# Kernel tuning notes

Hardware: AMD Instinct MI355X
Metric: run time of the kernel (lower is better)

Reference implementation:

```python
import jax, jax.numpy as jnp
import numpy as np

GN_EPS = 1e-5
NN_EPS = 1e-8


def _three_nn_interpolate(xyz1, xyz2, points2):
    # xyz1: (B,N,3), xyz2: (B,M,3), points2: (B,M,C) -> (B,N,C)
    src_sq = jnp.sum(xyz1 ** 2, axis=-1, keepdims=True)          # (B,N,1)
    dst_sq = jnp.sum(xyz2 ** 2, axis=-1)[:, None, :]             # (B,1,M)
    inner = jnp.einsum('bnd,bmd->bnm', xyz1, xyz2)               # (B,N,M)
    dist = src_sq - 2.0 * inner + dst_sq                         # (B,N,M)
    neg_d, idx = jax.lax.top_k(-dist, 3)                         # (B,N,3)
    d = -neg_d
    inv = 1.0 / (d + NN_EPS)
    w = inv / jnp.sum(inv, axis=-1, keepdims=True)               # (B,N,3)
    grouped = jax.vmap(lambda p, i: p[i])(points2, idx)          # (B,N,3,C)
    return jnp.sum(grouped * w[..., None], axis=2)               # (B,N,C)


def _group_norm(x, weight, bias, groups):
    # x: (B,C,N)
    B, C, N = x.shape
    xg = x.reshape(B, groups, C // groups, N)
    mu = jnp.mean(xg, axis=(2, 3), keepdims=True)
    var = jnp.var(xg, axis=(2, 3), keepdims=True)
    xg = (xg - mu) * jax.lax.rsqrt(var + GN_EPS)
    x = xg.reshape(B, C, N)
    return x * weight[None, :, None] + bias[None, :, None]


def setup_inputs() -> dict:
    key = jax.random.key(0)
    ks = jax.random.split(key, 10)
    B, N, M, C1, C2 = 8, 8192, 2048, 128, 256
    mlp = [256, 128]
    in_ch = C1 + C2
    inp = {
        'xyz1': jax.random.normal(ks[0], (B, N, 3), dtype=jnp.float32),
        'xyz2': jax.random.normal(ks[1], (B, M, 3), dtype=jnp.float32),
        'points1': jax.random.normal(ks[2], (B, N, C1), dtype=jnp.float32),
        'points2': jax.random.normal(ks[3], (B, M, C2), dtype=jnp.float32),
        'w0': jax.random.normal(ks[4], (mlp[0], in_ch), dtype=jnp.float32) * (1.0 / np.sqrt(in_ch)),
        'w1': jax.random.normal(ks[5], (mlp[1], mlp[0]), dtype=jnp.float32) * (1.0 / np.sqrt(mlp[0])),
        'gn0_w': jnp.ones((mlp[0],), dtype=jnp.float32),
        'gn0_b': jnp.zeros((mlp[0],), dtype=jnp.float32),
        'gn1_w': jnp.ones((mlp[1],), dtype=jnp.float32),
        'gn1_b': jnp.zeros((mlp[1],), dtype=jnp.float32),
    }
    return inp


def reference(xyz1, xyz2, points1, points2, w0, w1, gn0_w, gn0_b, gn1_w, gn1_b):
    interpolated = _three_nn_interpolate(xyz1, xyz2, points2)    # (B,N,C2)
    feat = jnp.concatenate([points1, interpolated], axis=-1)     # (B,N,C1+C2)
    # conv1d kernel size 1 == pointwise matmul; work in (B,C,N) layout for GN
    h = jnp.einsum('bnc,oc->bon', feat, w0)                      # (B,256,N)
    h = jax.nn.relu(_group_norm(h, gn0_w, gn0_b, groups=min(32, w0.shape[0])))
    h = jnp.einsum('bcn,oc->bon', h, w1)                         # (B,128,N)
    h = jax.nn.relu(_group_norm(h, gn1_w, gn1_b, groups=min(32, w1.shape[0])))
    return jnp.transpose(h, (0, 2, 1))                           # (B,N,128)
```

## Files before the change

kernel.cpp:

```cpp
#include <hip/hip_runtime.h>


#define DEVI __device__ __forceinline__

static constexpr int B  = 8;
static constexpr int N  = 8192;
static constexpr int M  = 2048;
static constexpr int C1 = 128;
static constexpr int C2 = 256;
static constexpr int CIN = C1 + C2;
static constexpr int H0 = 256;
static constexpr int H1 = 128;
static constexpr int BN = B * N;
static constexpr int NSEG = 8;
static constexpr int SEGL = M / NSEG;

typedef __bf16 bf16x8 __attribute__((ext_vector_type(8)));
typedef float  f32x4  __attribute__((ext_vector_type(4)));
typedef unsigned short ushort8v __attribute__((ext_vector_type(8)));

DEVI float bf2f(unsigned short u) {
    union { unsigned int i; float f; } v; v.i = ((unsigned int)u) << 16; return v.f;
}
DEVI unsigned short f2bf(float f) {
    union { float f; unsigned int i; } v; v.f = f;
    unsigned int x = v.i;
    return (unsigned short)((x + 0x7fffu + ((x >> 16) & 1u)) >> 16);
}
DEVI float ldin(const void* p, size_t i, int bf) {
    return bf ? bf2f(((const unsigned short*)p)[i]) : ((const float*)p)[i];
}
DEVI void ld8(const void* p, size_t i, int bf, float r[8]) {
    if (bf) {
        const ushort8v u = *(const ushort8v*)((const unsigned short*)p + i);
#pragma unroll
        for (int k = 0; k < 8; k++) r[k] = bf2f(u[k]);
    } else {
        const float4 a = *(const float4*)((const float*)p + i);
        const float4 b = *(const float4*)((const float*)p + i + 4);
        r[0] = a.x; r[1] = a.y; r[2] = a.z; r[3] = a.w;
        r[4] = b.x; r[5] = b.y; r[6] = b.z; r[7] = b.w;
    }
}
DEVI void ld8b(const unsigned short* p, size_t i, float r[8]) {
    const ushort8v u = *(const ushort8v*)(p + i);
#pragma unroll
    for (int k = 0; k < 8; k++) r[k] = bf2f(u[k]);
}

DEVI void gload16(const void* g, void* l) {
    __builtin_amdgcn_global_load_lds(
        (const __attribute__((address_space(1))) void*)g,
        (__attribute__((address_space(3))) void*)l, 16, 0, 0);
}

__global__ __launch_bounds__(64) void detect_dtype_kernel(const void* __restrict__ xyz1,
                                                          int* __restrict__ flag)
{
    const unsigned short* u = (const unsigned short*)xyz1;
    const int lane = threadIdx.x;
    const float av = fabsf(bf2f(u[2 * lane]));
    const bool in_range = (av >= 1e-4f && av <= 100.0f);
    const unsigned long long m = __ballot(in_range);
    if (lane == 0) flag[0] = (__popcll(m) >= 32) ? 1 : 0;
}

DEVI void cvt8(const void* src, unsigned short* dst, size_t j8, int bf) {
    if (bf) {
        *(ushort8v*)(dst + j8 * 8) = *(const ushort8v*)((const unsigned short*)src + j8 * 8);
    } else {
        float r[8];
        ld8(src, j8 * 8, 0, r);
        ushort8v o;
#pragma unroll
        for (int k = 0; k < 8; k++) o[k] = f2bf(r[k]);
        *(ushort8v*)(dst + j8 * 8) = o;
    }
}

__global__ __launch_bounds__(256) void prep_kernel(
    const void* __restrict__ w0, const void* __restrict__ w1,
    const void* __restrict__ p2, const void* __restrict__ xyz2,
    unsigned short* __restrict__ w0b, unsigned short* __restrict__ w1b,
    unsigned short* __restrict__ pb2,
    float4* __restrict__ c4, float* __restrict__ partz,
    const int* __restrict__ flag)
{
    const int bf = flag[0];
    constexpr int R0 = H0 * CIN / 8;
    constexpr int R1 = H1 * H0 / 8;
    constexpr int R2 = B * M;
    constexpr int R4 = B * M * C2 / 8;
    constexpr int R5 = 1024;
    constexpr int TOT = R0 + R1 + R2 + R4 + R5;
    for (int i = blockIdx.x * blockDim.x + threadIdx.x; i < TOT; i += gridDim.x * blockDim.x) {
        int j = i;
        if (j < R0) { cvt8(w0, w0b, j, bf); continue; }
        j -= R0;
        if (j < R1) { cvt8(w1, w1b, j, bf); continue; }
        j -= R1;
        if (j < R2) {
            const float x = ldin(xyz2, (size_t)j * 3 + 0, bf);
            const float y = ldin(xyz2, (size_t)j * 3 + 1, bf);
            const float z = ldin(xyz2, (size_t)j * 3 + 2, bf);
            const float sq = __fadd_rn(__fadd_rn(__fmul_rn(x, x), __fmul_rn(y, y)), __fmul_rn(z, z));
            c4[j] = make_float4(x, y, z, 0.5f * sq);
            continue;
        }
        j -= R2;
        if (j < R4) { cvt8(p2, pb2, j, bf); continue; }
        j -= R4;
        partz[j] = 0.f;
    }
}

__global__ __launch_bounds__(256) void knn3_split_kernel(
    const void* __restrict__ xyz1, const float4* __restrict__ c4,
    int* __restrict__ ci, const int* __restrict__ flag)
{
    const int bf = flag[0];
    const int tid = threadIdx.x;
    const int gid = blockIdx.x * 256 + tid;
    const int s = blockIdx.y;
    const int b = __builtin_amdgcn_readfirstlane(gid >> 13);

    const float x1 = ldin(xyz1, (size_t)gid * 3 + 0, bf);
    const float y1 = ldin(xyz1, (size_t)gid * 3 + 1, bf);
    const float z1 = ldin(xyz1, (size_t)gid * 3 + 2, bf);

    const float4* __restrict__ cand = c4 + b * M + s * SEGL;
    const int jbase = s * SEGL;
    constexpr int HALF = SEGL / 2;

    float a0 = 3.4e38f, a1 = 3.4e38f, a2 = 3.4e38f;
    int   ia0 = 0, ia1 = 0, ia2 = 0;
    float g0 = 3.4e38f, g1 = 3.4e38f, g2 = 3.4e38f;
    int   ig0 = 0, ig1 = 0, ig2 = 0;

#pragma unroll 4
    for (int j = 0; j < HALF; ++j) {
        const float4 pA = cand[j];
        const float4 pB = cand[j + HALF];
        const float sA = __builtin_fmaf(-x1, pA.x,
                          __builtin_fmaf(-y1, pA.y,
                           __builtin_fmaf(-z1, pA.z, pA.w)));
        const float sB = __builtin_fmaf(-x1, pB.x,
                          __builtin_fmaf(-y1, pB.y,
                           __builtin_fmaf(-z1, pB.z, pB.w)));
        {
            const int jn = jbase + j;
            const bool c0 = sA < a0;
            const float t1 = fmaxf(sA, a0); a0 = fminf(sA, a0);
            const int  tj1 = c0 ? ia0 : jn; ia0 = c0 ? jn : ia0;
            const bool c1 = t1 < a1;
            const float t2 = fmaxf(t1, a1); a1 = fminf(t1, a1);
            const int  tj2 = c1 ? ia1 : tj1; ia1 = c1 ? tj1 : ia1;
            const bool c2 = t2 < a2;
            a2 = fminf(t2, a2); ia2 = c2 ? tj2 : ia2;
        }
        {
            const int jn = jbase + HALF + j;
            const bool c0 = sB < g0;
            const float t1 = fmaxf(sB, g0); g0 = fminf(sB, g0);
            const int  tj1 = c0 ? ig0 : jn; ig0 = c0 ? jn : ig0;
            const bool c1 = t1 < g1;
            const float t2 = fmaxf(t1, g1); g1 = fminf(t1, g1);
            const int  tj2 = c1 ? ig1 : tj1; ig1 = c1 ? tj1 : ig1;
            const bool c2 = t2 < g2;
            g2 = fminf(t2, g2); ig2 = c2 ? tj2 : ig2;
        }
    }

    float mv[3] = { g0, g1, g2 };
    int   mi[3] = { ig0, ig1, ig2 };
#pragma unroll
    for (int k = 0; k < 3; ++k) {
        const float sv = mv[k]; const int jn = mi[k];
        const bool c0 = sv < a0;
        const float t1 = fmaxf(sv, a0); a0 = fminf(sv, a0);
        const int  tj1 = c0 ? ia0 : jn; ia0 = c0 ? jn : ia0;
        const bool c1 = t1 < a1;
        const float t2 = fmaxf(t1, a1); a1 = fminf(t1, a1);
        const int  tj2 = c1 ? ia1 : tj1; ia1 = c1 ? tj1 : ia1;
        const bool c2 = t2 < a2;
        a2 = fminf(t2, a2); ia2 = c2 ? tj2 : ia2;
    }

    ci[(size_t)(s * 3 + 0) * BN + gid] = ia0;
    ci[(size_t)(s * 3 + 1) * BN + gid] = ia1;
    ci[(size_t)(s * 3 + 2) * BN + gid] = ia2;
}

__global__ __launch_bounds__(512, 4) void gemm1_kernel(
    const void* __restrict__ p1, const unsigned short* __restrict__ pb2,
    const void* __restrict__ xyz1, const float4* __restrict__ c4,
    const int* __restrict__ ci,
    const unsigned short* __restrict__ W,
    unsigned short* __restrict__ h0, float2* __restrict__ part,
    const int* __restrict__ flag)
{
    constexpr int K = CIN;
    constexpr int COUT = H0;
    __shared__ __align__(16) char lds[81920];

    const int bf = flag[0];
    const int t = threadIdx.x;
    const int l = t & 63;
    const int w = t >> 6;
    const int qbase = blockIdx.x * 64;
    const int b = qbase >> 13;

    float* dd = (float*)(lds + 49152);
    int*   di = (int*)(lds + 55296);
    int*   sidx = (int*)(lds + 61440);
    float* sw = (float*)(lds + 62208);

    {
        const int ql = t >> 3;
        const int q  = qbase + ql;
        const int kk0 = (t & 7) * 3;
        const float x1 = ldin(xyz1, (size_t)q * 3 + 0, bf);
        const float y1 = ldin(xyz1, (size_t)q * 3 + 1, bf);
        const float z1 = ldin(xyz1, (size_t)q * 3 + 2, bf);
        const float sq1 = __fadd_rn(__fadd_rn(__fmul_rn(x1, x1), __fmul_rn(y1, y1)), __fmul_rn(z1, z1));
#pragma unroll
        for (int u = 0; u < 3; ++u) {
            const int k = kk0 + u;
            const int ix = ci[(size_t)k * BN + q];
            const float4 p = c4[b * M + ix];
            const float inner = __fadd_rn(__fadd_rn(__fmul_rn(x1, p.x), __fmul_rn(y1, p.y)),
                                          __fmul_rn(z1, p.z));
            const float pw2 = p.w + p.w;
            const float d = __fadd_rn(__fsub_rn(sq1, __fmul_rn(2.0f, inner)), pw2);
            dd[ql * 24 + k] = d;
            di[ql * 24 + k] = ix;
        }
    }
    __syncthreads();

    if (t < 64) {
        float bd0 = 3.4e38f, bd1 = 3.4e38f, bd2 = 3.4e38f;
        int   bi0 = 0x7fffffff, bi1 = 0x7fffffff, bi2 = 0x7fffffff;
#pragma unroll
        for (int k = 0; k < 24; ++k) {
            const float d  = dd[t * 24 + k];
            const int   ix = di[t * 24 + k];
            const bool lt2 = (d < bd2) || (d == bd2 && ix < bi2);
            if (lt2) {
                const bool lt0 = (d < bd0) || (d == bd0 && ix < bi0);
                const bool lt1 = (d < bd1) || (d == bd1 && ix < bi1);
                if (lt0)      { bd2 = bd1; bi2 = bi1; bd1 = bd0; bi1 = bi0; bd0 = d; bi0 = ix; }
                else if (lt1) { bd2 = bd1; bi2 = bi1; bd1 = d; bi1 = ix; }
                else          { bd2 = d; bi2 = ix; }
            }
        }
        const float v0 = 1.0f / (bd0 + 1e-8f);
        const float v1 = 1.0f / (bd1 + 1e-8f);
        const float v2 = 1.0f / (bd2 + 1e-8f);
        const float s = v0 + v1 + v2;
        sidx[t * 3 + 0] = bi0; sidx[t * 3 + 1] = bi1; sidx[t * 3 + 2] = bi2;
        sw[t * 3 + 0] = v0 / s; sw[t * 3 + 1] = v1 / s; sw[t * 3 + 2] = v2 / s;
    }
    __syncthreads();

#pragma unroll 1
    for (int it = 0; it < 6; ++it) {
        const int task = it * 512 + t;
        const int ql = task / 48;
        const int c8 = task % 48;
        const int c  = c8 * 8;
        float v[8];
        if (c < C1) {
            ld8(p1, (size_t)(qbase + ql) * C1 + c, bf, v);
        } else {
            const int c2 = c - C1;
            float t0[8], t1[8], t2[8];
            ld8b(pb2, (size_t)(b * M + sidx[ql * 3 + 0]) * C2 + c2, t0);
            ld8b(pb2, (size_t)(b * M + sidx[ql * 3 + 1]) * C2 + c2, t1);
            ld8b(pb2, (size_t)(b * M + sidx[ql * 3 + 2]) * C2 + c2, t2);
            const float w0v = sw[ql * 3 + 0], w1v = sw[ql * 3 + 1], w2v = sw[ql * 3 + 2];
#pragma unroll
            for (int k = 0; k < 8; k++) v[k] = w0v * t0[k] + w1v * t1[k] + w2v * t2[k];
        }
        ushort8v o;
#pragma unroll
        for (int k = 0; k < 8; k++) o[k] = f2bf(v[k]);
        *(ushort8v*)(lds + ql * 768 + ((c8 >> 3) << 7) + ((((c8 & 7) ^ (ql & 7)) << 4))) = o;
    }
    __syncthreads();

    const int srow  = l >> 3;
    const int sslot = l & 7;
    const int wr  = w >> 2;
    const int wc  = w & 3;
    const int rl  = l & 15;
    const int kq  = l >> 4;
    const int swz7 = l & 7;

    f32x4 acc[2][4];
#pragma unroll
    for (int i = 0; i < 2; i++)
#pragma unroll
        for (int j = 0; j < 4; j++) acc[i][j] = (f32x4)0.0f;

    int aoff[2], boff[4];
#pragma unroll
    for (int i = 0; i < 2; i++) aoff[i] = (wr * 32 + i * 16 + rl) * 768;
#pragma unroll
    for (int j = 0; j < 4; j++) boff[j] = 49152 + (wc * 64 + j * 16 + rl) * 128;

    constexpr int NT = K / 64;

#pragma unroll 1
    for (int tt = 0; tt < NT; ++tt) {
        const int k0 = tt * 64;
#pragma unroll
        for (int i = 0; i < 4; ++i) {
            const int cb = w * 4 + i;
            const int rb = cb * 8 + srow;
            const int ke = (sslot ^ (rb & 7)) << 3;
            gload16(W + ((size_t)rb * K + k0 + ke), lds + 49152 + cb * 1024);
        }
        __syncthreads();
#pragma unroll
        for (int ks = 0; ks < 2; ++ks) {
            const int akb = (tt << 7) + (((ks * 4 + kq) ^ swz7) << 4);
            const int bkb = (ks * 64 + kq * 16) ^ (swz7 << 4);
            bf16x8 af[2], bfr[4];
#pragma unroll
            for (int i = 0; i < 2; i++) af[i]  = *(const bf16x8*)(lds + aoff[i] + akb);
#pragma unroll
            for (int j = 0; j < 4; j++) bfr[j] = *(const bf16x8*)(lds + boff[j] + bkb);
#pragma unroll
            for (int i = 0; i < 2; i++)
#pragma unroll
                for (int j = 0; j < 4; j++)
                    acc[i][j] = __builtin_amdgcn_mfma_f32_16x16x32_bf16(af[i], bfr[j], acc[i][j], 0, 0, 0);
        }
        __syncthreads();
    }

    const int crow = qbase + wr * 32 + kq * 4;
    const int ccol = wc * 64 + rl;
    float gsum[4], gss[4];
#pragma unroll
    for (int j = 0; j < 4; j++) {
        float s = 0.f, ss = 0.f;
#pragma unroll
        for (int i = 0; i < 2; i++)
#pragma unroll
            for (int r = 0; r < 4; r++) {
                const unsigned short hb = f2bf(acc[i][j][r]);
                h0[(size_t)(crow + i * 16 + r) * COUT + ccol + j * 16] = hb;
                const float x = bf2f(hb);
                s += x; ss += x * x;
            }
        gsum[j] = s; gss[j] = ss;
    }
    __syncthreads();
    float2* sred = (float2*)lds;
    if (t < 32) sred[t] = make_float2(0.f, 0.f);
    __syncthreads();
#pragma unroll
    for (int j = 0; j < 4; j++) {
        const int g = wc * 8 + j * 2 + (rl >> 3);
        atomicAdd(&sred[g].x, gsum[j]);
        atomicAdd(&sred[g].y, gss[j]);
    }
    __syncthreads();
    if (t < 32) {
        atomicAdd(&part[b * 32 + t].x, sred[t].x);
        atomicAdd(&part[b * 32 + t].y, sred[t].y);
    }
}

__global__ __launch_bounds__(256) void gemm2_kernel(
    const unsigned short* __restrict__ h0, const float2* __restrict__ part0,
    const void* __restrict__ gw, const void* __restrict__ gb,
    const unsigned short* __restrict__ W,
    unsigned short* __restrict__ h1, float2* __restrict__ part1,
    const int* __restrict__ flag)
{
    constexpr int K = H0;
    constexpr int COUT = H1;
    __shared__ __align__(16) char lds[32768];
    __shared__ float2 stlds[32];

    const int bf = flag[0];
    const int tid = threadIdx.x;
    const int l   = tid & 63;
    const int w   = tid >> 6;
    const int rowBase = blockIdx.x * 128;
    const int b = rowBase >> 13;

    if (tid < 32) {
        const float2 p = part0[b * 32 + tid];
        const float cnt = (float)N * 8.0f;
        const float mu  = p.x / cnt;
        const float var = p.y / cnt - mu * mu;
        stlds[tid] = make_float2(mu, rsqrtf(var + 1e-5f));
    }
    __syncthreads();

    const int srow  = l >> 3;
    const int sslot = l & 7;

    f32x4 acc[4][4];
#pragma unroll
    for (int i = 0; i < 4; i++)
#pragma unroll
        for (int j = 0; j < 4; j++) acc[i][j] = (f32x4)0.0f;

    const int wr  = (tid >> 7) & 1;
    const int wc  = (tid >> 6) & 1;
    const int rl  = l & 15;
    const int kq  = l >> 4;
    const int swz = (l & 7) << 4;
    int aoff[4], boff[4];
#pragma unroll
    for (int i = 0; i < 4; i++) {
        aoff[i] = (wr * 64 + i * 16 + rl) * 128;
        boff[i] = 16384 + (wc * 64 + i * 16 + rl) * 128;
    }

    constexpr int NT = K / 64;

#pragma unroll 1
    for (int t = 0; t < NT; ++t) {
        const int k0 = t * 64;
#pragma unroll
        for (int i = 0; i < 4; ++i) {
            const int cb = w * 4 + i;
            const int r  = cb * 8 + srow;
            const int ke = (sslot ^ (r & 7)) << 3;
            gload16(W + ((size_t)r * K + k0 + ke), lds + 16384 + cb * 1024);
        }
#pragma unroll
        for (int i = 0; i < 4; ++i) {
            const int r = (w * 4 + i) * 8 + srow;
            const int kslot = sslot ^ (r & 7);
            const int c = k0 + (kslot << 3);
            const float2 ms = stlds[c >> 3];
            float gwv[8], gbv[8];
            ld8(gw, c, bf, gwv);
            ld8(gb, c, bf, gbv);
            const ushort8v hv = *(const ushort8v*)(h0 + (size_t)(rowBase + r) * H0 + c);
            ushort8v o;
#pragma unroll
            for (int k = 0; k < 8; k++) {
                const float x = bf2f(hv[k]);
                o[k] = f2bf(fmaxf((x - ms.x) * ms.y * gwv[k] + gbv[k], 0.f));
            }
            *(ushort8v*)(lds + r * 128 + (sslot << 4)) = o;
        }
        __syncthreads();
#pragma unroll
        for (int ks = 0; ks < 2; ++ks) {
            const int kb = (ks * 64 + kq * 16) ^ swz;
            bf16x8 af[4], bfr[4];
#pragma unroll
            for (int i = 0; i < 4; i++) af[i]  = *(const bf16x8*)(lds + aoff[i] + kb);
#pragma unroll
            for (int j = 0; j < 4; j++) bfr[j] = *(const bf16x8*)(lds + boff[j] + kb);
#pragma unroll
            for (int i = 0; i < 4; i++)
#pragma unroll
                for (int j = 0; j < 4; j++)
                    acc[i][j] = __builtin_amdgcn_mfma_f32_16x16x32_bf16(af[i], bfr[j], acc[i][j], 0, 0, 0);
        }
        __syncthreads();
    }

    const int crow = rowBase + wr * 64 + kq * 4;
    const int ccol = wc * 64 + rl;
    float gsum[4], gss[4];
#pragma unroll
    for (int j = 0; j < 4; j++) {
        float s = 0.f, ss = 0.f;
#pragma unroll
        for (int i = 0; i < 4; i++)
#pragma unroll
            for (int r = 0; r < 4; r++) {
                const unsigned short hb = f2bf(acc[i][j][r]);
                h1[(size_t)(crow + i * 16 + r) * COUT + ccol + j * 16] = hb;
                const float x = bf2f(hb);
                s += x; ss += x * x;
            }
        gsum[j] = s; gss[j] = ss;
    }
    __syncthreads();
    float2* sred = (float2*)lds;
    if (tid < 32) sred[tid] = make_float2(0.f, 0.f);
    __syncthreads();
#pragma unroll
    for (int j = 0; j < 4; j++) {
        const int g = wc * 16 + j * 4 + (rl >> 2);
        atomicAdd(&sred[g].x, gsum[j]);
        atomicAdd(&sred[g].y, gss[j]);
    }
    __syncthreads();
    if (tid < 32) {
        atomicAdd(&part1[b * 32 + tid].x, sred[tid].x);
        atomicAdd(&part1[b * 32 + tid].y, sred[tid].y);
    }
}

__global__ __launch_bounds__(256) void gn_norm_relu_kernel(
    const unsigned short* __restrict__ h, const float2* __restrict__ part1,
    const void* __restrict__ gw, const void* __restrict__ gb,
    void* __restrict__ out, const int* __restrict__ flag)
{
    constexpr int C = H1;
    constexpr int cpg = 4;
    constexpr int C4 = C >> 2;
    constexpr int total4 = BN * C / 4;

    __shared__ float2 stlds[256];
    {
        const float2 p = part1[threadIdx.x];
        const float cnt = (float)N * (float)cpg;
        const float mu  = p.x / cnt;
        const float var = p.y / cnt - mu * mu;
        stlds[threadIdx.x] = make_float2(mu, rsqrtf(var + 1e-5f));
    }
    __syncthreads();

    const int bf = flag[0];
    for (int i4 = blockIdx.x * blockDim.x + threadIdx.x; i4 < total4; i4 += gridDim.x * blockDim.x) {
        const int c = (i4 % C4) * 4;
        const int p = i4 / C4;
        const int b = p >> 13;
        const float2 ms = stlds[b * 32 + c / cpg];
        const ushort4 hv = *(const ushort4*)(h + (size_t)i4 * 4);
        float r[4] = { bf2f(hv.x), bf2f(hv.y), bf2f(hv.z), bf2f(hv.w) };
#pragma unroll
        for (int k = 0; k < 4; k++) {
            const float gwv = ldin(gw, c + k, bf);
            const float gbv = ldin(gb, c + k, bf);
            r[k] = fmaxf((r[k] - ms.x) * ms.y * gwv + gbv, 0.f);
        }
        if (bf) {
            ushort4 o;
            o.x = f2bf(r[0]); o.y = f2bf(r[1]); o.z = f2bf(r[2]); o.w = f2bf(r[3]);
            *(ushort4*)((unsigned short*)out + (size_t)i4 * 4) = o;
        } else {
            float4 o; o.x = r[0]; o.y = r[1]; o.z = r[2]; o.w = r[3];
            *(float4*)((float*)out + (size_t)i4 * 4) = o;
        }
    }
}

extern "C" void kernel_launch(void* const* d_in, const int* in_sizes, int n_in,
                              void* d_out, int out_size, void* d_ws, size_t ws_size,
                              hipStream_t stream)
{
    const void* xyz1    = d_in[0];
    const void* xyz2    = d_in[1];
    const void* points1 = d_in[2];
    const void* points2 = d_in[3];
    const void* w0      = d_in[4];
    const void* w1      = d_in[5];
    const void* gn0w    = d_in[6];
    const void* gn0b    = d_in[7];
    const void* gn1w    = d_in[8];
    const void* gn1b    = d_in[9];

    char* ws = (char*)d_ws;
    unsigned short* h0     = (unsigned short*)ws;
    unsigned short* h1     = (unsigned short*)(ws + 33554432);
    unsigned short* w0b    = (unsigned short*)(ws + 50331648);
    unsigned short* w1b    = (unsigned short*)(ws + 50528256);
    unsigned short* pb2    = (unsigned short*)(ws + 50593792);
    float4*         c4     = (float4*)(ws + 58982400);
    int*            ci     = (int*)(ws + 59244544);
    float2*         part0  = (float2*)(ws + 65536000);
    float2*         part1  = (float2*)(ws + 65538048);
    int*            flag   = (int*)(ws + 65540096);

    detect_dtype_kernel<<<1, 64, 0, stream>>>(xyz1, flag);

    prep_kernel<<<1024, 256, 0, stream>>>(w0, w1, points2, xyz2,
                                          w0b, w1b, pb2, c4, (float*)part0, flag);

    {
        dim3 g(BN / 256, NSEG);
        knn3_split_kernel<<<g, 256, 0, stream>>>(xyz1, c4, ci, flag);
    }

    gemm1_kernel<<<BN / 64, 512, 0, stream>>>(points1, pb2, xyz1, c4, ci,
                                              w0b, h0, part0, flag);

    gemm2_kernel<<<BN / 128, 256, 0, stream>>>(h0, part0, gn0w, gn0b, w1b, h1,
                                               part1, flag);

    gn_norm_relu_kernel<<<1024, 256, 0, stream>>>(h1, part1, gn1w, gn1b, d_out, flag);
}
```

Before: 294.1 us.

## Gather fp32 points2 directly, inline dtype detection, widen gemm1 blocks to 1024 threads

Drops the prep-pass conversion of points2 to bf16. gemm1 now gathers and weights the three neighbours straight from the original fp32 buffer, which avoids a full read and write pass over points2 but doubles the bytes fetched per gather. The separate dtype-detection kernel is removed and each kernel runs the ballot check itself, saving one launch. gemm1 is retiled to 1024 threads (16 waves, each holding a 16x64 output tile), which halves per-wave accumulator registers and raises the thread count available for the gather, and the prep grid is shrunk to match its smaller workload.

```diff
diff --git a/kernel.cpp b/kernel.cpp
--- a/kernel.cpp
+++ b/kernel.cpp
@@ -42,27 +42,20 @@
         r[4] = b.x; r[5] = b.y; r[6] = b.z; r[7] = b.w;
     }
 }
-DEVI void ld8b(const unsigned short* p, size_t i, float r[8]) {
-    const ushort8v u = *(const ushort8v*)(p + i);
-#pragma unroll
-    for (int k = 0; k < 8; k++) r[k] = bf2f(u[k]);
+
+DEVI int detect_bf(const void* xyz1) {
+    const unsigned short* u = (const unsigned short*)xyz1;
+    const int lane = threadIdx.x & 63;
+    const float av = fabsf(bf2f(u[2 * lane]));
+    const bool in_range = (av >= 1e-4f && av <= 100.0f);
+    const unsigned long long m = __ballot(in_range);
+    return (__popcll(m) >= 32) ? 1 : 0;
 }
 
 DEVI void gload16(const void* g, void* l) {
     __builtin_amdgcn_global_load_lds(
         (const __attribute__((address_space(1))) void*)g,
         (__attribute__((address_space(3))) void*)l, 16, 0, 0);
-}
-
-__global__ __launch_bounds__(64) void detect_dtype_kernel(const void* __restrict__ xyz1,
-                                                          int* __restrict__ flag)
-{
-    const unsigned short* u = (const unsigned short*)xyz1;
-    const int lane = threadIdx.x;
-    const float av = fabsf(bf2f(u[2 * lane]));
-    const bool in_range = (av >= 1e-4f && av <= 100.0f);
-    const unsigned long long m = __ballot(in_range);
-    if (lane == 0) flag[0] = (__popcll(m) >= 32) ? 1 : 0;
 }
 
 DEVI void cvt8(const void* src, unsigned short* dst, size_t j8, int bf) {
@@ -80,19 +73,16 @@
 
 __global__ __launch_bounds__(256) void prep_kernel(
     const void* __restrict__ w0, const void* __restrict__ w1,
-    const void* __restrict__ p2, const void* __restrict__ xyz2,
+    const void* __restrict__ xyz1, const void* __restrict__ xyz2,
     unsigned short* __restrict__ w0b, unsigned short* __restrict__ w1b,
-    unsigned short* __restrict__ pb2,
-    float4* __restrict__ c4, float* __restrict__ partz,
-    const int* __restrict__ flag)
+    float4* __restrict__ c4, float* __restrict__ partz)
 {
-    const int bf = flag[0];
+    const int bf = detect_bf(xyz1);
     constexpr int R0 = H0 * CIN / 8;
     constexpr int R1 = H1 * H0 / 8;
     constexpr int R2 = B * M;
-    constexpr int R4 = B * M * C2 / 8;
     constexpr int R5 = 1024;
-    constexpr int TOT = R0 + R1 + R2 + R4 + R5;
+    constexpr int TOT = R0 + R1 + R2 + R5;
     for (int i = blockIdx.x * blockDim.x + threadIdx.x; i < TOT; i += gridDim.x * blockDim.x) {
         int j = i;
         if (j < R0) { cvt8(w0, w0b, j, bf); continue; }
@@ -108,17 +98,15 @@
             continue;
         }
         j -= R2;
-        if (j < R4) { cvt8(p2, pb2, j, bf); continue; }
-        j -= R4;
         partz[j] = 0.f;
     }
 }
 
 __global__ __launch_bounds__(256) void knn3_split_kernel(
     const void* __restrict__ xyz1, const float4* __restrict__ c4,
-    int* __restrict__ ci, const int* __restrict__ flag)
+    int* __restrict__ ci)
 {
-    const int bf = flag[0];
+    const int bf = detect_bf(xyz1);
     const int tid = threadIdx.x;
     const int gid = blockIdx.x * 256 + tid;
     const int s = blockIdx.y;
@@ -191,19 +179,18 @@
     ci[(size_t)(s * 3 + 2) * BN + gid] = ia2;
 }
 
-__global__ __launch_bounds__(512, 4) void gemm1_kernel(
-    const void* __restrict__ p1, const unsigned short* __restrict__ pb2,
+__global__ __launch_bounds__(1024, 8) void gemm1_kernel(
+    const void* __restrict__ p1, const void* __restrict__ p2,
     const void* __restrict__ xyz1, const float4* __restrict__ c4,
     const int* __restrict__ ci,
     const unsigned short* __restrict__ W,
-    unsigned short* __restrict__ h0, float2* __restrict__ part,
-    const int* __restrict__ flag)
+    unsigned short* __restrict__ h0, float2* __restrict__ part)
 {
     constexpr int K = CIN;
     constexpr int COUT = H0;
     __shared__ __align__(16) char lds[81920];
 
-    const int bf = flag[0];
+    const int bf = detect_bf(xyz1);
     const int t = threadIdx.x;
     const int l = t & 63;
     const int w = t >> 6;
@@ -215,7 +202,7 @@
     int*   sidx = (int*)(lds + 61440);
     float* sw = (float*)(lds + 62208);
 
-    {
+    if (t < 512) {
         const int ql = t >> 3;
         const int q  = qbase + ql;
         const int kk0 = (t & 7) * 3;
@@ -264,8 +251,8 @@
     __syncthreads();
 
 #pragma unroll 1
-    for (int it = 0; it < 6; ++it) {
-        const int task = it * 512 + t;
+    for (int it = 0; it < 3; ++it) {
+        const int task = it * 1024 + t;
         const int ql = task / 48;
         const int c8 = task % 48;
         const int c  = c8 * 8;
@@ -275,9 +262,9 @@
         } else {
             const int c2 = c - C1;
             float t0[8], t1[8], t2[8];
-            ld8b(pb2, (size_t)(b * M + sidx[ql * 3 + 0]) * C2 + c2, t0);
-            ld8b(pb2, (size_t)(b * M + sidx[ql * 3 + 1]) * C2 + c2, t1);
-            ld8b(pb2, (size_t)(b * M + sidx[ql * 3 + 2]) * C2 + c2, t2);
+            ld8(p2, (size_t)(b * M + sidx[ql * 3 + 0]) * C2 + c2, bf, t0);
+            ld8(p2, (size_t)(b * M + sidx[ql * 3 + 1]) * C2 + c2, bf, t1);
+            ld8(p2, (size_t)(b * M + sidx[ql * 3 + 2]) * C2 + c2, bf, t2);
             const float w0v = sw[ql * 3 + 0], w1v = sw[ql * 3 + 1], w2v = sw[ql * 3 + 2];
 #pragma unroll
             for (int k = 0; k < 8; k++) v[k] = w0v * t0[k] + w1v * t1[k] + w2v * t2[k];
@@ -297,15 +284,12 @@
     const int kq  = l >> 4;
     const int swz7 = l & 7;
 
-    f32x4 acc[2][4];
-#pragma unroll
-    for (int i = 0; i < 2; i++)
-#pragma unroll
-        for (int j = 0; j < 4; j++) acc[i][j] = (f32x4)0.0f;
-
-    int aoff[2], boff[4];
-#pragma unroll
-    for (int i = 0; i < 2; i++) aoff[i] = (wr * 32 + i * 16 + rl) * 768;
+    f32x4 acc[4];
+#pragma unroll
+    for (int j = 0; j < 4; j++) acc[j] = (f32x4)0.0f;
+
+    const int aoff = (wr * 16 + rl) * 768;
+    int boff[4];
 #pragma unroll
     for (int j = 0; j < 4; j++) boff[j] = 49152 + (wc * 64 + j * 16 + rl) * 128;
 
@@ -315,8 +299,8 @@
     for (int tt = 0; tt < NT; ++tt) {
         const int k0 = tt * 64;
 #pragma unroll
-        for (int i = 0; i < 4; ++i) {
-            const int cb = w * 4 + i;
+        for (int i = 0; i < 2; ++i) {
+            const int cb = w * 2 + i;
             const int rb = cb * 8 + srow;
             const int ke = (sslot ^ (rb & 7)) << 3;
             gload16(W + ((size_t)rb * K + k0 + ke), lds + 49152 + cb * 1024);
@@ -326,35 +310,30 @@
         for (int ks = 0; ks < 2; ++ks) {
             const int akb = (tt << 7) + (((ks * 4 + kq) ^ swz7) << 4);
             const int bkb = (ks * 64 + kq * 16) ^ (swz7 << 4);
-            bf16x8 af[2], bfr[4];
-#pragma unroll
-            for (int i = 0; i < 2; i++) af[i]  = *(const bf16x8*)(lds + aoff[i] + akb);
+            const bf16x8 af = *(const bf16x8*)(lds + aoff + akb);
+            bf16x8 bfr[4];
 #pragma unroll
             for (int j = 0; j < 4; j++) bfr[j] = *(const bf16x8*)(lds + boff[j] + bkb);
 #pragma unroll
-            for (int i = 0; i < 2; i++)
-#pragma unroll
-                for (int j = 0; j < 4; j++)
-                    acc[i][j] = __builtin_amdgcn_mfma_f32_16x16x32_bf16(af[i], bfr[j], acc[i][j], 0, 0, 0);
+            for (int j = 0; j < 4; j++)
+                acc[j] = __builtin_amdgcn_mfma_f32_16x16x32_bf16(af, bfr[j], acc[j], 0, 0, 0);
         }
         __syncthreads();
     }
 
-    const int crow = qbase + wr * 32 + kq * 4;
+    const int crow = qbase + wr * 16 + kq * 4;
     const int ccol = wc * 64 + rl;
     float gsum[4], gss[4];
 #pragma unroll
     for (int j = 0; j < 4; j++) {
         float s = 0.f, ss = 0.f;
 #pragma unroll
-        for (int i = 0; i < 2; i++)
-#pragma unroll
-            for (int r = 0; r < 4; r++) {
-                const unsigned short hb = f2bf(acc[i][j][r]);
-                h0[(size_t)(crow + i * 16 + r) * COUT + ccol + j * 16] = hb;
-                const float x = bf2f(hb);
-                s += x; ss += x * x;
-            }
+        for (int r = 0; r < 4; r++) {
+            const unsigned short hb = f2bf(acc[j][r]);
+            h0[(size_t)(crow + r) * COUT + ccol + j * 16] = hb;
+            const float x = bf2f(hb);
+            s += x; ss += x * x;
+        }
         gsum[j] = s; gss[j] = ss;
     }
     __syncthreads();
@@ -377,16 +356,15 @@
 __global__ __launch_bounds__(256) void gemm2_kernel(
     const unsigned short* __restrict__ h0, const float2* __restrict__ part0,
     const void* __restrict__ gw, const void* __restrict__ gb,
-    const unsigned short* __restrict__ W,
-    unsigned short* __restrict__ h1, float2* __restrict__ part1,
-    const int* __restrict__ flag)
+    const unsigned short* __restrict__ W, const void* __restrict__ xyz1,
+    unsigned short* __restrict__ h1, float2* __restrict__ part1)
 {
     constexpr int K = H0;
     constexpr int COUT = H1;
     __shared__ __align__(16) char lds[32768];
     __shared__ float2 stlds[32];
 
-    const int bf = flag[0];
+    const int bf = detect_bf(xyz1);
     const int tid = threadIdx.x;
     const int l   = tid & 63;
     const int w   = tid >> 6;
@@ -508,7 +486,7 @@
 __global__ __launch_bounds__(256) void gn_norm_relu_kernel(
     const unsigned short* __restrict__ h, const float2* __restrict__ part1,
     const void* __restrict__ gw, const void* __restrict__ gb,
-    void* __restrict__ out, const int* __restrict__ flag)
+    const void* __restrict__ xyz1, void* __restrict__ out)
 {
     constexpr int C = H1;
     constexpr int cpg = 4;
@@ -523,9 +501,9 @@
         const float var = p.y / cnt - mu * mu;
         stlds[threadIdx.x] = make_float2(mu, rsqrtf(var + 1e-5f));
     }
-    __syncthreads();
-
-    const int bf = flag[0];
+    const int bf = detect_bf(xyz1);
+    __syncthreads();
+
     for (int i4 = blockIdx.x * blockDim.x + threadIdx.x; i4 < total4; i4 += gridDim.x * blockDim.x) {
         const int c = (i4 % C4) * 4;
         const int p = i4 / C4;
@@ -570,28 +548,24 @@
     unsigned short* h1     = (unsigned short*)(ws + 33554432);
     unsigned short* w0b    = (unsigned short*)(ws + 50331648);
     unsigned short* w1b    = (unsigned short*)(ws + 50528256);
-    unsigned short* pb2    = (unsigned short*)(ws + 50593792);
-    float4*         c4     = (float4*)(ws + 58982400);
-    int*            ci     = (int*)(ws + 59244544);
-    float2*         part0  = (float2*)(ws + 65536000);
-    float2*         part1  = (float2*)(ws + 65538048);
-    int*            flag   = (int*)(ws + 65540096);
-
-    detect_dtype_kernel<<<1, 64, 0, stream>>>(xyz1, flag);
-
-    prep_kernel<<<1024, 256, 0, stream>>>(w0, w1, points2, xyz2,
-                                          w0b, w1b, pb2, c4, (float*)part0, flag);
+    float4*         c4     = (float4*)(ws + 50593792);
+    int*            ci     = (int*)(ws + 50855936);
+    float2*         part0  = (float2*)(ws + 57147392);
+    float2*         part1  = (float2*)(ws + 57149440);
+
+    prep_kernel<<<144, 256, 0, stream>>>(w0, w1, xyz1, xyz2, w0b, w1b,
+                                         c4, (float*)part0);
 
     {
         dim3 g(BN / 256, NSEG);
-        knn3_split_kernel<<<g, 256, 0, stream>>>(xyz1, c4, ci, flag);
-    }
-
-    gemm1_kernel<<<BN / 64, 512, 0, stream>>>(points1, pb2, xyz1, c4, ci,
-                                              w0b, h0, part0, flag);
-
-    gemm2_kernel<<<BN / 128, 256, 0, stream>>>(h0, part0, gn0w, gn0b, w1b, h1,
-                                               part1, flag);
-
-    gn_norm_relu_kernel<<<1024, 256, 0, stream>>>(h1, part1, gn1w, gn1b, d_out, flag);
-}
+        knn3_split_kernel<<<g, 256, 0, stream>>>(xyz1, c4, ci);
+    }
+
+    gemm1_kernel<<<BN / 64, 1024, 0, stream>>>(points1, points2, xyz1, c4, ci,
+                                               w0b, h0, part0);
+
+    gemm2_kernel<<<BN / 128, 256, 0, stream>>>(h0, part0, gn0w, gn0b, w1b, xyz1,
+                                               h1, part1);
+
+    gn_norm_relu_kernel<<<1024, 256, 0, stream>>>(h1, part1, gn1w, gn1b, xyz1, d_out);
+}
```

Result: slower. 320.0 us (+8.8%).

## Inline dtype detection per kernel and halve gemm2 row tile

Applied to the files above, without the earlier changes.

Drops the single-wave dtype-detection kernel and recomputes the bf16 flag inside every kernel with a wave ballot over the first xyz1 values, removing one launch and a serial dependency. gemm2 now uses 64-row tiles instead of 128, doubling its grid and cutting its LDS and accumulator footprint to improve occupancy. The final normalize kernel's grid is also doubled. In exchange every thread does a few extra global loads and a ballot, and the smaller gemm2 tile reloads the W tile more often.

```diff
diff --git a/kernel.cpp b/kernel.cpp
--- a/kernel.cpp
+++ b/kernel.cpp
@@ -48,21 +48,19 @@
     for (int k = 0; k < 8; k++) r[k] = bf2f(u[k]);
 }
 
+DEVI int detect_bf(const void* xyz1) {
+    const unsigned short* u = (const unsigned short*)xyz1;
+    const int lane = threadIdx.x & 63;
+    const float av = fabsf(bf2f(u[2 * lane]));
+    const bool in_range = (av >= 1e-4f && av <= 100.0f);
+    const unsigned long long m = __ballot(in_range);
+    return (__popcll(m) >= 32) ? 1 : 0;
+}
+
 DEVI void gload16(const void* g, void* l) {
     __builtin_amdgcn_global_load_lds(
         (const __attribute__((address_space(1))) void*)g,
         (__attribute__((address_space(3))) void*)l, 16, 0, 0);
-}
-
-__global__ __launch_bounds__(64) void detect_dtype_kernel(const void* __restrict__ xyz1,
-                                                          int* __restrict__ flag)
-{
-    const unsigned short* u = (const unsigned short*)xyz1;
-    const int lane = threadIdx.x;
-    const float av = fabsf(bf2f(u[2 * lane]));
-    const bool in_range = (av >= 1e-4f && av <= 100.0f);
-    const unsigned long long m = __ballot(in_range);
-    if (lane == 0) flag[0] = (__popcll(m) >= 32) ? 1 : 0;
 }
 
 DEVI void cvt8(const void* src, unsigned short* dst, size_t j8, int bf) {
@@ -80,13 +78,13 @@
 
 __global__ __launch_bounds__(256) void prep_kernel(
     const void* __restrict__ w0, const void* __restrict__ w1,
-    const void* __restrict__ p2, const void* __restrict__ xyz2,
+    const void* __restrict__ p2,
+    const void* __restrict__ xyz1, const void* __restrict__ xyz2,
     unsigned short* __restrict__ w0b, unsigned short* __restrict__ w1b,
     unsigned short* __restrict__ pb2,
-    float4* __restrict__ c4, float* __restrict__ partz,
-    const int* __restrict__ flag)
+    float4* __restrict__ c4, float* __restrict__ partz)
 {
-    const int bf = flag[0];
+    const int bf = detect_bf(xyz1);
     constexpr int R0 = H0 * CIN / 8;
     constexpr int R1 = H1 * H0 / 8;
     constexpr int R2 = B * M;
@@ -116,9 +114,9 @@
 
 __global__ __launch_bounds__(256) void knn3_split_kernel(
     const void* __restrict__ xyz1, const float4* __restrict__ c4,
-    int* __restrict__ ci, const int* __restrict__ flag)
+    int* __restrict__ ci)
 {
-    const int bf = flag[0];
+    const int bf = detect_bf(xyz1);
     const int tid = threadIdx.x;
     const int gid = blockIdx.x * 256 + tid;
     const int s = blockIdx.y;
@@ -196,14 +194,13 @@
     const void* __restrict__ xyz1, const float4* __restrict__ c4,
     const int* __restrict__ ci,
     const unsigned short* __restrict__ W,
-    unsigned short* __restrict__ h0, float2* __restrict__ part,
-    const int* __restrict__ flag)
+    unsigned short* __restrict__ h0, float2* __restrict__ part)
 {
     constexpr int K = CIN;
     constexpr int COUT = H0;
     __shared__ __align__(16) char lds[81920];
 
-    const int bf = flag[0];
+    const int bf = detect_bf(xyz1);
     const int t = threadIdx.x;
     const int l = t & 63;
     const int w = t >> 6;
@@ -377,20 +374,19 @@
 __global__ __launch_bounds__(256) void gemm2_kernel(
     const unsigned short* __restrict__ h0, const float2* __restrict__ part0,
     const void* __restrict__ gw, const void* __restrict__ gb,
-    const unsigned short* __restrict__ W,
-    unsigned short* __restrict__ h1, float2* __restrict__ part1,
-    const int* __restrict__ flag)
+    const unsigned short* __restrict__ W, const void* __restrict__ xyz1,
+    unsigned short* __restrict__ h1, float2* __restrict__ part1)
 {
     constexpr int K = H0;
     constexpr int COUT = H1;
-    __shared__ __align__(16) char lds[32768];
+    __shared__ __align__(16) char lds[24576];
     __shared__ float2 stlds[32];
 
-    const int bf = flag[0];
+    const int bf = detect_bf(xyz1);
     const int tid = threadIdx.x;
     const int l   = tid & 63;
     const int w   = tid >> 6;
-    const int rowBase = blockIdx.x * 128;
+    const int rowBase = blockIdx.x * 64;
     const int b = rowBase >> 13;
 
     if (tid < 32) {
@@ -405,9 +401,9 @@
     const int srow  = l >> 3;
     const int sslot = l & 7;
 
-    f32x4 acc[4][4];
-#pragma unroll
-    for (int i = 0; i < 4; i++)
+    f32x4 acc[2][4];
+#pragma unroll
+    for (int i = 0; i < 2; i++)
 #pragma unroll
         for (int j = 0; j < 4; j++) acc[i][j] = (f32x4)0.0f;
 
@@ -416,12 +412,11 @@
     const int rl  = l & 15;
     const int kq  = l >> 4;
     const int swz = (l & 7) << 4;
-    int aoff[4], boff[4];
-#pragma unroll
-    for (int i = 0; i < 4; i++) {
-        aoff[i] = (wr * 64 + i * 16 + rl) * 128;
-        boff[i] = 16384 + (wc * 64 + i * 16 + rl) * 128;
-    }
+    int aoff[2], boff[4];
+#pragma unroll
+    for (int i = 0; i < 2; i++) aoff[i] = (wr * 32 + i * 16 + rl) * 128;
+#pragma unroll
+    for (int j = 0; j < 4; j++) boff[j] = 8192 + (wc * 64 + j * 16 + rl) * 128;
 
     constexpr int NT = K / 64;
 
@@ -433,11 +428,11 @@
             const int cb = w * 4 + i;
             const int r  = cb * 8 + srow;
             const int ke = (sslot ^ (r & 7)) << 3;
-            gload16(W + ((size_t)r * K + k0 + ke), lds + 16384 + cb * 1024);
-        }
-#pragma unroll
-        for (int i = 0; i < 4; ++i) {
-            const int r = (w * 4 + i) * 8 + srow;
+            gload16(W + ((size_t)r * K + k0 + ke), lds + 8192 + cb * 1024);
+        }
+#pragma unroll
+        for (int i = 0; i < 2; ++i) {
+            const int r = (w * 2 + i) * 8 + srow;
             const int kslot = sslot ^ (r & 7);
             const int c = k0 + (kslot << 3);
             const float2 ms = stlds[c >> 3];
@@ -457,13 +452,13 @@
 #pragma unroll
         for (int ks = 0; ks < 2; ++ks) {
             const int kb = (ks * 64 + kq * 16) ^ swz;
-            bf16x8 af[4], bfr[4];
-#pragma unroll
-            for (int i = 0; i < 4; i++) af[i]  = *(const bf16x8*)(lds + aoff[i] + kb);
+            bf16x8 af[2], bfr[4];
+#pragma unroll
+            for (int i = 0; i < 2; i++) af[i]  = *(const bf16x8*)(lds + aoff[i] + kb);
 #pragma unroll
             for (int j = 0; j < 4; j++) bfr[j] = *(const bf16x8*)(lds + boff[j] + kb);
 #pragma unroll
-            for (int i = 0; i < 4; i++)
+            for (int i = 0; i < 2; i++)
 #pragma unroll
                 for (int j = 0; j < 4; j++)
                     acc[i][j] = __builtin_amdgcn_mfma_f32_16x16x32_bf16(af[i], bfr[j], acc[i][j], 0, 0, 0);
@@ -471,14 +466,14 @@
         __syncthreads();
     }
 
-    const int crow = rowBase + wr * 64 + kq * 4;
+    const int crow = rowBase + wr * 32 + kq * 4;
     const int ccol = wc * 64 + rl;
     float gsum[4], gss[4];
 #pragma unroll
     for (int j = 0; j < 4; j++) {
         float s = 0.f, ss = 0.f;
 #pragma unroll
-        for (int i = 0; i < 4; i++)
+        for (int i = 0; i < 2; i++)
 #pragma unroll
             for (int r = 0; r < 4; r++) {
                 const unsigned short hb = f2bf(acc[i][j][r]);
@@ -508,7 +503,7 @@
 __global__ __launch_bounds__(256) void gn_norm_relu_kernel(
     const unsigned short* __restrict__ h, const float2* __restrict__ part1,
     const void* __restrict__ gw, const void* __restrict__ gb,
-    void* __restrict__ out, const int* __restrict__ flag)
+    const void* __restrict__ xyz1, void* __restrict__ out)
 {
     constexpr int C = H1;
     constexpr int cpg = 4;
@@ -523,9 +518,9 @@
         const float var = p.y / cnt - mu * mu;
         stlds[threadIdx.x] = make_float2(mu, rsqrtf(var + 1e-5f));
     }
-    __syncthreads();
-
-    const int bf = flag[0];
+    const int bf = detect_bf(xyz1);
+    __syncthreads();
+
     for (int i4 = blockIdx.x * blockDim.x + threadIdx.x; i4 < total4; i4 += gridDim.x * blockDim.x) {
         const int c = (i4 % C4) * 4;
         const int p = i4 / C4;
@@ -575,23 +570,20 @@
     int*            ci     = (int*)(ws + 59244544);
     float2*         part0  = (float2*)(ws + 65536000);
     float2*         part1  = (float2*)(ws + 65538048);
-    int*            flag   = (int*)(ws + 65540096);
-
-    detect_dtype_kernel<<<1, 64, 0, stream>>>(xyz1, flag);
-
-    prep_kernel<<<1024, 256, 0, stream>>>(w0, w1, points2, xyz2,
-                                          w0b, w1b, pb2, c4, (float*)part0, flag);
+
+    prep_kernel<<<1024, 256, 0, stream>>>(w0, w1, points2, xyz1, xyz2,
+                                          w0b, w1b, pb2, c4, (float*)part0);
 
     {
         dim3 g(BN / 256, NSEG);
-        knn3_split_kernel<<<g, 256, 0, stream>>>(xyz1, c4, ci, flag);
+        knn3_split_kernel<<<g, 256, 0, stream>>>(xyz1, c4, ci);
     }
 
     gemm1_kernel<<<BN / 64, 512, 0, stream>>>(points1, pb2, xyz1, c4, ci,
-                                              w0b, h0, part0, flag);
-
-    gemm2_kernel<<<BN / 128, 256, 0, stream>>>(h0, part0, gn0w, gn0b, w1b, h1,
-                                               part1, flag);
-
-    gn_norm_relu_kernel<<<1024, 256, 0, stream>>>(h1, part1, gn1w, gn1b, d_out, flag);
-}
+                                              w0b, h0, part0);
+
+    gemm2_kernel<<<BN / 64, 256, 0, stream>>>(h0, part0, gn0w, gn0b, w1b, xyz1,
+                                              h1, part1);
+
+    gn_norm_relu_kernel<<<2048, 256, 0, stream>>>(h1, part1, gn1w, gn1b, xyz1, d_out);
+}
```

Result: no change. 299.5 us (+1.8%).
